# Kernel optimization log

Hardware: AMD Instinct MI355X
Metric: run time of the kernel (lower is better)

## Reference

```python
import jax, jax.numpy as jnp
import numpy as np

CL1_K = 25
CL2_K = 25


def cheb_stack(L, x0, K):
    # x0: (V, M) -> (K, V, M) Chebyshev basis T_k(L) x0
    if K == 1:
        return x0[None]
    x1 = L @ x0
    if K == 2:
        return jnp.stack([x0, x1])

    def step(carry, _):
        xm1, xm2 = carry
        xk = 2.0 * (L @ xm1) - xm2
        return (xk, xm1), xk

    _, rest = jax.lax.scan(step, (x1, x0), None, length=K - 2)
    return jnp.concatenate([x0[None], x1[None], rest], axis=0)


def graph_conv(x, L, W, b, K):
    # x: (B, C, V) -> (B, Fout, V); matches torch Graph_Conv permute/view logic
    B, C, V = x.shape
    x0 = x.transpose(2, 1, 0).reshape(V, C * B)
    xs = cheb_stack(L, x0, K)                              # (K, V, C*B)
    xs = xs.reshape(K, V, C, B).transpose(3, 1, 2, 0)      # (B, V, C, K)
    xs = xs.reshape(B * V, C * K)
    y = xs @ W.T + b                                       # (B*V, Fout)
    return y.reshape(B, V, -1).transpose(0, 2, 1)


def maxpool4(x):
    B, C, V = x.shape
    return x.reshape(B, C, V // 4, 4).max(axis=-1)


def setup_inputs() -> dict:
    key = jax.random.key(0)
    ks = jax.random.split(key, 10)
    B, C, V, Vp = 32, 16, 4000, 4096
    CL1_F, CL2_F, FC_F = 64, 128, 10
    x = jax.random.normal(ks[0], (B, C, V), dtype=jnp.float32)
    perm = jax.random.permutation(ks[1], Vp)
    # rescaled Laplacians, scaled for stable 25-step recurrence
    L1 = jax.random.normal(ks[2], (Vp, Vp), dtype=jnp.float32) * (0.3 / np.sqrt(Vp))
    L2 = jax.random.normal(ks[3], (Vp // 4, Vp // 4), dtype=jnp.float32) * (0.3 / np.sqrt(Vp // 4))
    W1 = jax.random.normal(ks[4], (CL1_F, C * CL1_K), dtype=jnp.float32) * np.sqrt(2.0 / (C * CL1_K + CL1_F))
    b1 = jnp.zeros((CL1_F,), dtype=jnp.float32)
    W2 = jax.random.normal(ks[5], (CL2_F, CL1_F * CL2_K), dtype=jnp.float32) * np.sqrt(2.0 / (CL1_F * CL2_K + CL2_F))
    b2 = jnp.zeros((CL2_F,), dtype=jnp.float32)
    FC_IN = CL2_F * Vp // 16
    Wfc = jax.random.normal(ks[6], (FC_F, FC_IN), dtype=jnp.float32) * np.sqrt(2.0 / (FC_IN + FC_F))
    bfc = jnp.zeros((FC_F,), dtype=jnp.float32)
    return {"x": x, "perm": perm, "L1": L1, "L2": L2, "W1": W1, "b1": b1,
            "W2": W2, "b2": b2, "Wfc": Wfc, "bfc": bfc}


def reference(x, perm, L1, L2, W1, b1, W2, b2, Wfc, bfc):
    # BatchNorm1d(affine=False), training-mode batch statistics
    mu = x.mean(axis=(0, 2), keepdims=True)
    var = x.var(axis=(0, 2), keepdims=True)
    x = (x - mu) / jnp.sqrt(var + 1e-5)
    # Permute: zero-pad vertices to len(perm), then index
    B, C, V = x.shape
    Vp = perm.shape[0]
    x = jnp.pad(x, ((0, 0), (0, 0), (0, Vp - V)))[:, :, perm]
    x = jax.nn.relu(graph_conv(x, L1, W1, b1, CL1_K))
    x = maxpool4(x)
    x = jax.nn.relu(graph_conv(x, L2, W2, b2, CL2_K))
    x = maxpool4(x)
    x = x.reshape(B, -1)
    # dropout in eval mode (identity)
    return x @ Wfc.T + bfc
```

## Files before the change

kernel.cpp:

```cpp
#include <hip/hip_runtime.h>

typedef _Float16 half8 __attribute__((ext_vector_type(8)));
typedef _Float16 half4 __attribute__((ext_vector_type(4)));
typedef float f32x4 __attribute__((ext_vector_type(4)));

__device__ __forceinline__ void gload_lds16(const void* g, void* l) {
  __builtin_amdgcn_global_load_lds((const __attribute__((address_space(1))) void*)g,
                                   (__attribute__((address_space(3))) void*)l, 16, 0, 0);
}

__global__ __launch_bounds__(256) void k_bn_partial(const float* __restrict__ x,
                                                    float* __restrict__ part) {
  const int c = blockIdx.x & 15;
  const int seg = blockIdx.x >> 4;
  const int t = threadIdx.x;
  float s = 0.f, s2 = 0.f;
  for (int b = 0; b < 32; ++b) {
    const float* row = x + (size_t)(b * 16 + c) * 4000 + seg * 500;
    for (int v = t; v < 500; v += 256) {
      float val = row[v];
      s += val;
      s2 += val * val;
    }
  }
#pragma unroll
  for (int off = 32; off > 0; off >>= 1) {
    s += __shfl_down(s, off);
    s2 += __shfl_down(s2, off);
  }
  __shared__ float rs_[4], rs2_[4];
  if ((t & 63) == 0) { rs_[t >> 6] = s; rs2_[t >> 6] = s2; }
  __syncthreads();
  if (t == 0) {
    part[c * 8 + seg] = rs_[0] + rs_[1] + rs_[2] + rs_[3];
    part[128 + c * 8 + seg] = rs2_[0] + rs2_[1] + rs2_[2] + rs2_[3];
  }
}

__global__ void k_bn_final(const float* __restrict__ part, float* __restrict__ musig) {
  const int c = threadIdx.x;
  if (c < 16) {
    float S = 0.f, S2 = 0.f;
#pragma unroll
    for (int seg = 0; seg < 8; ++seg) {
      S += part[c * 8 + seg];
      S2 += part[128 + c * 8 + seg];
    }
    const float inv = 1.f / 128000.f;
    float mu = S * inv;
    float var = S2 * inv - mu * mu;
    musig[c] = mu;
    musig[16 + c] = rsqrtf(var + 1e-5f);
  }
}

__global__ __launch_bounds__(256) void k_build_x0(const float* __restrict__ x,
                                                  const int* __restrict__ perm,
                                                  const float* __restrict__ musig,
                                                  _Float16* __restrict__ X0) {
  const int idx = blockIdx.x * 256 + threadIdx.x;
  const int v = idx & 4095;
  const int m = idx >> 12;
  const int b = m & 31;
  const int c = m >> 5;
  const int pv = perm[v];
  float val = 0.f;
  if (pv < 4000)
    val = (x[((size_t)(b * 16 + c)) * 4000 + pv] - musig[c]) * musig[16 + c] * 0.0625f;
  X0[idx] = (_Float16)val;
}

__global__ __launch_bounds__(256) void k_cvt_f16(const float* __restrict__ s,
                                                 _Float16* __restrict__ d, int n) {
  const int i = (blockIdx.x * 256 + threadIdx.x) * 4;
  if (i >= n) return;
  f32x4 v = *(const f32x4*)(s + i);
  half4 h;
  h[0] = (_Float16)v[0]; h[1] = (_Float16)v[1];
  h[2] = (_Float16)v[2]; h[3] = (_Float16)v[3];
  *(half4*)(d + i) = h;
}

__global__ __launch_bounds__(256) void k_zero(_Float16* __restrict__ p, int n8) {
  const int i = blockIdx.x * 256 + threadIdx.x;
  if (i < n8) *(half8*)(p + (size_t)i * 8) = half8{};
}

__global__ __launch_bounds__(256) void k_prep_w(const float* __restrict__ W,
                                                _Float16* __restrict__ Wp,
                                                int F, int shiftC, int kround) {
  const int idx = blockIdx.x * 256 + threadIdx.x;
  const int CS = 1 << shiftC;
  const int KPtot = kround * CS;
  if (idx >= F * KPtot) return;
  const int f = idx / KPtot;
  const int rem = idx - f * KPtot;
  const int k = rem >> shiftC;
  const int c = rem & (CS - 1);
  float v = 0.f;
  if (k < 25) v = W[(size_t)f * (CS * 25) + c * 25 + k];
  Wp[idx] = (_Float16)v;
}

__global__ __launch_bounds__(256, 2) void k_cheb1b(const _Float16* __restrict__ Xprev,
                                                   const _Float16* __restrict__ Lm,
                                                   _Float16* __restrict__ P) {
  __shared__ _Float16 lds[3][8192];
  const int t = threadIdx.x;
  const int lane = t & 63;
  const int ln = lane & 15;
  const int g = lane >> 4;
  const int w = t >> 6;
  const int wm = w >> 1, wn = w & 1;
  const int bid = blockIdx.x;
  const int kq = bid & 3;
  const int bx = (bid >> 2) & 31;
  const int by = bid >> 7;
  const int v0 = bx * 128, m0 = by * 128;
  const size_t rs = 8192;

  const char* Ag = (const char*)Xprev + (size_t)m0 * rs + kq * 2048;
  const char* Bg = (const char*)Lm + (size_t)v0 * rs + kq * 2048;

  f32x4 acc[4][4] = {};

  auto stage = [&](int buf, int tt) {
    char* A = (char*)&lds[buf][0];
    char* B = (char*)&lds[buf][4096];
#pragma unroll
    for (int j = 0; j < 2; ++j) {
      const int ch = j * 256 + t;
      const int row = ch >> 2, c8 = ch & 3;
      const size_t so = (size_t)row * rs + tt * 64 + ((c8 ^ ((row >> 1) & 3)) << 4);
      gload_lds16(Ag + so, A + ch * 16);
      gload_lds16(Bg + so, B + ch * 16);
    }
  };

  stage(0, 0);
  stage(1, 1);
  asm volatile("s_waitcnt vmcnt(4)" ::: "memory");
  asm volatile("s_barrier" ::: "memory");

  for (int tt = 0; tt < 32; ++tt) {
    const int cur = tt % 3;
    const char* A = (const char*)&lds[cur][0];
    const char* B = A + 8192;
    half8 a[4], b[4];
#pragma unroll
    for (int mi = 0; mi < 4; ++mi) {
      const int ar = wm * 64 + mi * 16 + ln;
      a[mi] = *(const half8*)(A + ar * 64 + ((g ^ ((ar >> 1) & 3)) << 4));
    }
#pragma unroll
    for (int ni = 0; ni < 4; ++ni) {
      const int br = wn * 64 + ni * 16 + ln;
      b[ni] = *(const half8*)(B + br * 64 + ((g ^ ((br >> 1) & 3)) << 4));
    }
    if (tt + 2 < 32) {
      stage((tt + 2) % 3, tt + 2);
      asm volatile("s_waitcnt vmcnt(4)" ::: "memory");
    } else {
      asm volatile("s_waitcnt vmcnt(0)" ::: "memory");
    }
    asm volatile("s_barrier" ::: "memory");
    asm volatile("s_waitcnt lgkmcnt(0)" ::: "memory");
    __builtin_amdgcn_sched_barrier(0);
    __builtin_amdgcn_s_setprio(1);
#pragma unroll
    for (int mi = 0; mi < 4; ++mi)
#pragma unroll
      for (int ni = 0; ni < 4; ++ni)
        acc[mi][ni] = __builtin_amdgcn_mfma_f32_16x16x32_f16(a[mi], b[ni], acc[mi][ni], 0, 0, 0);
    __builtin_amdgcn_s_setprio(0);
    asm volatile("s_barrier" ::: "memory");
  }

  _Float16* Pq = P + (size_t)kq * 2097152;
#pragma unroll
  for (int mi = 0; mi < 4; ++mi) {
#pragma unroll
    for (int ni = 0; ni < 4; ++ni) {
      const int vv = v0 + wn * 64 + ni * 16 + ln;
      const int mmb = m0 + wm * 64 + mi * 16 + g * 4;
#pragma unroll
      for (int r = 0; r < 4; ++r)
        Pq[(size_t)(mmb + r) * 4096 + vv] = (_Float16)acc[mi][ni][r];
    }
  }
}

__global__ __launch_bounds__(256) void k_cheb_red4(const _Float16* __restrict__ P,
                                                   const _Float16* __restrict__ Xm2,
                                                   _Float16* __restrict__ Xout,
                                                   float alpha, float beta) {
  const size_t i = ((size_t)blockIdx.x * 256 + threadIdx.x) * 8;
  float s[8] = {};
#pragma unroll
  for (int p = 0; p < 4; ++p) {
    half8 v = *(const half8*)(P + (size_t)p * 2097152 + i);
#pragma unroll
    for (int j = 0; j < 8; ++j) s[j] += (float)v[j];
  }
  half8 xm2 = {};
  if (beta != 0.f) xm2 = *(const half8*)(Xm2 + i);
  half8 o;
#pragma unroll
  for (int j = 0; j < 8; ++j) o[j] = (_Float16)(alpha * s[j] - beta * (float)xm2[j]);
  *(half8*)(Xout + i) = o;
}

__global__ __launch_bounds__(256, 2) void k_cheb2(const _Float16* __restrict__ Xprev,
                                                  const _Float16* __restrict__ Lm,
                                                  const _Float16* __restrict__ Xm2,
                                                  _Float16* __restrict__ Xout,
                                                  float alpha, float beta) {
  __shared__ _Float16 lds[3][8192];
  const int t = threadIdx.x;
  const int lane = t & 63;
  const int ln = lane & 15;
  const int g = lane >> 4;
  const int g16 = g << 4;
  const int w = t >> 6;
  const int wm = w >> 1, wn = w & 1;
  const int bx = blockIdx.x & 15;
  const int by = blockIdx.x >> 4;
  const int v0 = bx * 64, m0 = by * 64;
  const size_t rs = 2048;

  const char* Ag = (const char*)Xprev + (size_t)m0 * rs;
  const char* Bg = (const char*)Lm + (size_t)v0 * rs;

  f32x4 acc[2][2] = {};

  auto stageHalf = [&](int buf, int tt, int half) {
    const char* src = (half == 0) ? Ag : Bg;
    char* dst0 = (char*)&lds[buf][0] + half * 8192;
#pragma unroll
    for (int j = 0; j < 2; ++j) {
      const int idx = j * 256 + t;
      const int row = idx >> 3, c8 = idx & 7;
      gload_lds16(src + (size_t)row * rs + tt * 128 + ((c8 ^ (row & 7)) << 4),
                  dst0 + idx * 16);
    }
  };

  stageHalf(0, 0, 0); stageHalf(0, 0, 1);
  stageHalf(1, 1, 0); stageHalf(1, 1, 1);
  asm volatile("s_waitcnt vmcnt(4)" ::: "memory");
  asm volatile("s_barrier" ::: "memory");

  for (int tt = 0; tt < 16; ++tt) {
    const int cur = tt % 3;
    const int nxt = (tt + 2) % 3;
    const char* A = (const char*)&lds[cur][0];
    const char* B = A + 8192;
    half8 a[2][2], b[2][2];
#pragma unroll
    for (int kk = 0; kk < 2; ++kk) {
#pragma unroll
      for (int mi = 0; mi < 2; ++mi) {
        const int ar = wm * 32 + mi * 16 + ln;
        a[kk][mi] = *(const half8*)(A + ar * 128 + ((kk * 64 + g16) ^ ((ar & 7) << 4)));
      }
#pragma unroll
      for (int ni = 0; ni < 2; ++ni) {
        const int br = wn * 32 + ni * 16 + ln;
        b[kk][ni] = *(const half8*)(B + br * 128 + ((kk * 64 + g16) ^ ((br & 7) << 4)));
      }
    }
    if (tt + 2 < 16) {
      stageHalf(nxt, tt + 2, 0);
      stageHalf(nxt, tt + 2, 1);
      asm volatile("s_waitcnt vmcnt(4)" ::: "memory");
    } else {
      asm volatile("s_waitcnt vmcnt(0)" ::: "memory");
    }
    asm volatile("s_barrier" ::: "memory");
    asm volatile("s_waitcnt lgkmcnt(0)" ::: "memory");
    __builtin_amdgcn_sched_barrier(0);
    __builtin_amdgcn_s_setprio(1);
#pragma unroll
    for (int kk = 0; kk < 2; ++kk)
#pragma unroll
      for (int mi = 0; mi < 2; ++mi)
#pragma unroll
        for (int ni = 0; ni < 2; ++ni)
          acc[mi][ni] = __builtin_amdgcn_mfma_f32_16x16x32_f16(a[kk][mi], b[kk][ni],
                                                               acc[mi][ni], 0, 0, 0);
    __builtin_amdgcn_s_setprio(0);
    asm volatile("s_barrier" ::: "memory");
  }

#pragma unroll
  for (int mi = 0; mi < 2; ++mi) {
#pragma unroll
    for (int ni = 0; ni < 2; ++ni) {
      const int vv = v0 + wn * 32 + ni * 16 + ln;
      const int mmb = m0 + wm * 32 + mi * 16 + g * 4;
#pragma unroll
      for (int r = 0; r < 4; ++r) {
        const size_t idx = (size_t)(mmb + r) * 1024 + vv;
        float val = alpha * acc[mi][ni][r];
        if (beta != 0.f) val -= (float)Xm2[idx];
        Xout[idx] = (_Float16)val;
      }
    }
  }
}

template <int FT>
__global__ __launch_bounds__(256, 2) void k_dense(const _Float16* __restrict__ Wp,
                                                  const _Float16* __restrict__ XS,
                                                  const float* __restrict__ bias,
                                                  float* __restrict__ Yt,
                                                  int Vv, int shiftC, int nsteps,
                                                  int Ntot, float ascale, float bscale) {
  __shared__ _Float16 Alds[2][FT * 64];
  __shared__ _Float16 Blds[2][64 * 64];
  const int t = threadIdx.x;
  const int lane = t & 63;
  const int g = lane >> 4;
  const int w = t >> 6;
  const int n0 = blockIdx.x * 64;
  const int b = n0 / Vv;
  const int vb = n0 % Vv;
  const int Kp = nsteps * 64;
  const int cmask = (1 << shiftC) - 1;
  const size_t plane = 2097152;

  f32x4 acc[FT / 16] = {};

  auto stage = [&](int buf, int s) {
    const int q0 = s * 64;
    char* A = (char*)&Alds[buf][0];
    char* B = (char*)&Blds[buf][0];
#pragma unroll
    for (int j = 0; j < FT / 32; ++j) {
      const int ch = j * 256 + t;
      const int f = ch >> 3, c8 = ch & 7;
      gload_lds16((const char*)Wp + ((size_t)f * Kp + q0) * 2 + ((c8 ^ (f & 7)) << 4),
                  A + ch * 16);
    }
#pragma unroll
    for (int j = 0; j < 2; ++j) {
      const int ch = j * 256 + t;
      const int q = ch >> 3, c8 = ch & 7;
      const int qq = q0 + q;
      const int k = qq >> shiftC, c = qq & cmask;
      const int sz = (q >> 3) & 7;
      gload_lds16((const char*)XS + ((size_t)k * plane + (size_t)(c * 32 + b) * Vv + vb) * 2 +
                      ((c8 ^ sz) << 4),
                  B + ch * 16);
    }
  };

  stage(0, 0);

  for (int s = 0; s < nsteps; ++s) {
    const int cur = s & 1;
    if (s + 1 < nsteps) {
      stage(cur ^ 1, s + 1);
      if constexpr (FT == 64) {
        asm volatile("s_waitcnt vmcnt(4)" ::: "memory");
      } else {
        asm volatile("s_waitcnt vmcnt(6)" ::: "memory");
      }
    } else {
      asm volatile("s_waitcnt vmcnt(0)" ::: "memory");
    }
    asm volatile("s_barrier" ::: "memory");
    const _Float16* A = &Alds[cur][0];
    const _Float16* B = &Blds[cur][0];
#pragma unroll
    for (int kk = 0; kk < 2; ++kk) {
      half8 bf;
      const int c = lane & 15;
#pragma unroll
      for (int j = 0; j < 8; ++j) {
        const int q = kk * 32 + g * 8 + j;
        const int sz = (q >> 3) & 7;
        bf[j] = B[q * 64 + ((w * 16 + c) ^ (sz << 3))];
      }
#pragma unroll
      for (int mi = 0; mi < FT / 16; ++mi) {
        const int ar = mi * 16 + c;
        half8 af = *(const half8*)((const char*)A + ar * 128 +
                                   ((kk * 64 + g * 16) ^ ((ar & 7) << 4)));
        acc[mi] = __builtin_amdgcn_mfma_f32_16x16x32_f16(af, bf, acc[mi], 0, 0, 0);
      }
    }
    asm volatile("s_barrier" ::: "memory");
  }

  const int n = n0 + w * 16 + (lane & 15);
#pragma unroll
  for (int mi = 0; mi < FT / 16; ++mi) {
#pragma unroll
    for (int r = 0; r < 4; ++r) {
      const int f = mi * 16 + g * 4 + r;
      Yt[(size_t)f * Ntot + n] = fmaxf(ascale * acc[mi][r] + bscale * bias[f], 0.f);
    }
  }
}

__global__ __launch_bounds__(256) void k_pool1(const float* __restrict__ Yt,
                                               _Float16* __restrict__ X2) {
  const int idx = blockIdx.x * 256 + threadIdx.x;
  const int v2 = idx & 1023;
  const int rest = idx >> 10;
  const int b = rest & 31;
  const int f = rest >> 5;
  f32x4 q = *(const f32x4*)(Yt + (size_t)f * 131072 + b * 4096 + v2 * 4);
  float mx = fmaxf(fmaxf(q[0], q[1]), fmaxf(q[2], q[3]));
  X2[(size_t)(f * 32 + b) * 1024 + v2] = (_Float16)(mx * 0.015625f);
}

__global__ __launch_bounds__(256) void k_pool2(const float* __restrict__ Yt,
                                               float* __restrict__ p2) {
  const int idx = blockIdx.x * 256 + threadIdx.x;
  const int v3 = idx & 255;
  const int rest = idx >> 8;
  const int f = rest & 127;
  const int b = rest >> 7;
  f32x4 q = *(const f32x4*)(Yt + (size_t)f * 32768 + b * 1024 + v3 * 4);
  float mx = fmaxf(fmaxf(q[0], q[1]), fmaxf(q[2], q[3]));
  p2[(size_t)b * 32768 + f * 256 + v3] = mx;
}

__global__ __launch_bounds__(256) void k_fc_part(const float* __restrict__ p2,
                                                 const float* __restrict__ Wfc,
                                                 float* __restrict__ partF) {
  const int b = blockIdx.x >> 3;
  const int seg = blockIdx.x & 7;
  const int t = threadIdx.x;
  const int lane = t & 63;
  const int w = t >> 6;
  const int base = seg * 4096;
  float acc[10];
#pragma unroll
  for (int o = 0; o < 10; ++o) acc[o] = 0.f;
  const float* pb = p2 + (size_t)b * 32768 + base;
  for (int i = t; i < 4096; i += 256) {
    float p = pb[i];
#pragma unroll
    for (int o = 0; o < 10; ++o) acc[o] += p * Wfc[(size_t)o * 32768 + base + i];
  }
#pragma unroll
  for (int off = 32; off > 0; off >>= 1)
#pragma unroll
    for (int o = 0; o < 10; ++o) acc[o] += __shfl_down(acc[o], off);
  __shared__ float rws[10][4];
  if (lane == 0) {
#pragma unroll
    for (int o = 0; o < 10; ++o) rws[o][w] = acc[o];
  }
  __syncthreads();
  if (t < 10) partF[blockIdx.x * 10 + t] =
      rws[t][0] + rws[t][1] + rws[t][2] + rws[t][3];
}

__global__ void k_fc_final(const float* __restrict__ partF,
                           const float* __restrict__ bfc,
                           float* __restrict__ out) {
  const int t = threadIdx.x;
  if (t < 320) {
    const int b = t / 10, o = t - b * 10;
    float s = 0.f;
#pragma unroll
    for (int seg = 0; seg < 8; ++seg) s += partF[(b * 8 + seg) * 10 + o];
    out[b * 10 + o] = 64.f * s + bfc[o];
  }
}

extern "C" void kernel_launch(void* const* d_in, const int* in_sizes, int n_in,
                              void* d_out, int out_size, void* d_ws, size_t ws_size,
                              hipStream_t stream) {
  (void)in_sizes; (void)n_in; (void)out_size; (void)ws_size;
  const float* x = (const float*)d_in[0];
  const int* perm = (const int*)d_in[1];
  const float* L1 = (const float*)d_in[2];
  const float* L2 = (const float*)d_in[3];
  const float* W1 = (const float*)d_in[4];
  const float* b1 = (const float*)d_in[5];
  const float* W2 = (const float*)d_in[6];
  const float* b2 = (const float*)d_in[7];
  const float* Wfc = (const float*)d_in[8];
  const float* bfc = (const float*)d_in[9];
  float* out = (float*)d_out;

  char* ws = (char*)d_ws;
  size_t off = 0;
  auto alloc = [&](size_t bytes) {
    char* p = ws + off;
    off += (bytes + 255) & ~(size_t)255;
    return p;
  };
  _Float16* L1h = (_Float16*)alloc(16777216ull * 2);
  _Float16* L2h = (_Float16*)alloc(1048576ull * 2);
  _Float16* W1p = (_Float16*)alloc(64ull * 448 * 2);
  _Float16* W2p = (_Float16*)alloc(128ull * 1664 * 2);
  float* part = (float*)alloc(256 * 4);
  float* musig = (float*)alloc(32 * 4);
  float* partF = (float*)alloc(2560 * 4);
  _Float16* XS = (_Float16*)alloc(28ull * 2097152 * 2);
  float* Yt = (float*)alloc(64ull * 131072 * 4);
  float* p2 = (float*)alloc(32ull * 128 * 256 * 4);
  _Float16* Pq = (_Float16*)Yt;

  const size_t plane = 2097152;

  k_cvt_f16<<<16384, 256, 0, stream>>>(L1, L1h, 16777216);
  k_cvt_f16<<<1024, 256, 0, stream>>>(L2, L2h, 1048576);
  k_prep_w<<<112, 256, 0, stream>>>(W1, W1p, 64, 4, 28);
  k_prep_w<<<832, 256, 0, stream>>>(W2, W2p, 128, 6, 26);
  k_zero<<<3072, 256, 0, stream>>>(XS + 25 * plane, 786432);
  k_bn_partial<<<128, 256, 0, stream>>>(x, part);
  k_bn_final<<<1, 64, 0, stream>>>(part, musig);
  k_build_x0<<<8192, 256, 0, stream>>>(x, perm, musig, XS);

  for (int k = 1; k < 25; ++k) {
    k_cheb1b<<<512, 256, 0, stream>>>(XS + (size_t)(k - 1) * plane, L1h, Pq);
    k_cheb_red4<<<1024, 256, 0, stream>>>(
        Pq, XS + (size_t)(k >= 2 ? k - 2 : 0) * plane, XS + (size_t)k * plane,
        (k == 1) ? 1.f : 2.f, (k == 1) ? 0.f : 1.f);
  }
  k_dense<64><<<dim3(2048, 1), 256, 0, stream>>>(W1p, XS, b1, Yt, 4096, 4, 7,
                                                 131072, 16.f, 1.f);
  k_pool1<<<8192, 256, 0, stream>>>(Yt, XS);
  for (int k = 1; k < 25; ++k) {
    k_cheb2<<<512, 256, 0, stream>>>(
        XS + (size_t)(k - 1) * plane, L2h,
        XS + (size_t)(k >= 2 ? k - 2 : 0) * plane, XS + (size_t)k * plane,
        (k == 1) ? 1.f : 2.f, (k == 1) ? 0.f : 1.f);
  }
  k_dense<128><<<dim3(512, 1), 256, 0, stream>>>(W2p, XS, b2, Yt, 1024, 6, 26,
                                                 32768, 1.f, 0.015625f);
  k_pool2<<<4096, 256, 0, stream>>>(Yt, p2);
  k_fc_part<<<256, 256, 0, stream>>>(p2, Wfc, partF);
  k_fc_final<<<1, 320, 0, stream>>>(partF, bfc, out);
}
```

Baseline: 1.188 ms.

## Fuse maxpool into dense epilogue and deepen cheb1 LDS pipeline to four stages

The dense kernels now apply the 4-way max pool in their epilogue with lane shuffles and write pooled outputs directly. This removes the separate pool kernels and the full-resolution fp32 intermediate writes and reads. The layer-1 pooled output goes to a new extra plane so it doesn't clobber plane 0 while it is still being read. Separately, the cheb1 GEMM uses four LDS buffers with a prefetch distance of three to hide more global-load latency, at the cost of more shared memory per block.

```diff
diff --git a/kernel.cpp b/kernel.cpp
--- a/kernel.cpp
+++ b/kernel.cpp
@@ -105,7 +105,7 @@
 __global__ __launch_bounds__(256, 2) void k_cheb1b(const _Float16* __restrict__ Xprev,
                                                    const _Float16* __restrict__ Lm,
                                                    _Float16* __restrict__ P) {
-  __shared__ _Float16 lds[3][8192];
+  __shared__ _Float16 lds[4][8192];
   const int t = threadIdx.x;
   const int lane = t & 63;
   const int ln = lane & 15;
@@ -139,11 +139,12 @@
 
   stage(0, 0);
   stage(1, 1);
-  asm volatile("s_waitcnt vmcnt(4)" ::: "memory");
+  stage(2, 2);
+  asm volatile("s_waitcnt vmcnt(8)" ::: "memory");
   asm volatile("s_barrier" ::: "memory");
 
   for (int tt = 0; tt < 32; ++tt) {
-    const int cur = tt % 3;
+    const int cur = tt & 3;
     const char* A = (const char*)&lds[cur][0];
     const char* B = A + 8192;
     half8 a[4], b[4];
@@ -157,8 +158,10 @@
       const int br = wn * 64 + ni * 16 + ln;
       b[ni] = *(const half8*)(B + br * 64 + ((g ^ ((br >> 1) & 3)) << 4));
     }
-    if (tt + 2 < 32) {
-      stage((tt + 2) % 3, tt + 2);
+    if (tt + 3 < 32) {
+      stage((tt + 3) & 3, tt + 3);
+      asm volatile("s_waitcnt vmcnt(8)" ::: "memory");
+    } else if (tt + 2 < 32) {
       asm volatile("s_waitcnt vmcnt(4)" ::: "memory");
     } else {
       asm volatile("s_waitcnt vmcnt(0)" ::: "memory");
@@ -309,13 +312,13 @@
   }
 }
 
-template <int FT>
+template <int FT, int MODE>
 __global__ __launch_bounds__(256, 2) void k_dense(const _Float16* __restrict__ Wp,
                                                   const _Float16* __restrict__ XS,
                                                   const float* __restrict__ bias,
-                                                  float* __restrict__ Yt,
+                                                  void* __restrict__ outp,
                                                   int Vv, int shiftC, int nsteps,
-                                                  int Ntot, float ascale, float bscale) {
+                                                  int k0plane, float ascale, float bscale) {
   __shared__ _Float16 Alds[2][FT * 64];
   __shared__ _Float16 Blds[2][64 * 64];
   const int t = threadIdx.x;
@@ -347,7 +350,9 @@
       const int ch = j * 256 + t;
       const int q = ch >> 3, c8 = ch & 7;
       const int qq = q0 + q;
-      const int k = qq >> shiftC, c = qq & cmask;
+      int k = qq >> shiftC;
+      const int c = qq & cmask;
+      if (k == 0) k = k0plane;
       const int sz = (q >> 3) & 7;
       gload_lds16((const char*)XS + ((size_t)k * plane + (size_t)(c * 32 + b) * Vv + vb) * 2 +
                       ((c8 ^ sz) << 4),
@@ -393,39 +398,27 @@
     asm volatile("s_barrier" ::: "memory");
   }
 
-  const int n = n0 + w * 16 + (lane & 15);
+  const int v = vb + w * 16 + (lane & 15);
+  const bool writer = (lane & 3) == 0;
 #pragma unroll
   for (int mi = 0; mi < FT / 16; ++mi) {
 #pragma unroll
     for (int r = 0; r < 4; ++r) {
       const int f = mi * 16 + g * 4 + r;
-      Yt[(size_t)f * Ntot + n] = fmaxf(ascale * acc[mi][r] + bscale * bias[f], 0.f);
-    }
-  }
-}
-
-__global__ __launch_bounds__(256) void k_pool1(const float* __restrict__ Yt,
-                                               _Float16* __restrict__ X2) {
-  const int idx = blockIdx.x * 256 + threadIdx.x;
-  const int v2 = idx & 1023;
-  const int rest = idx >> 10;
-  const int b = rest & 31;
-  const int f = rest >> 5;
-  f32x4 q = *(const f32x4*)(Yt + (size_t)f * 131072 + b * 4096 + v2 * 4);
-  float mx = fmaxf(fmaxf(q[0], q[1]), fmaxf(q[2], q[3]));
-  X2[(size_t)(f * 32 + b) * 1024 + v2] = (_Float16)(mx * 0.015625f);
-}
-
-__global__ __launch_bounds__(256) void k_pool2(const float* __restrict__ Yt,
-                                               float* __restrict__ p2) {
-  const int idx = blockIdx.x * 256 + threadIdx.x;
-  const int v3 = idx & 255;
-  const int rest = idx >> 8;
-  const int f = rest & 127;
-  const int b = rest >> 7;
-  f32x4 q = *(const f32x4*)(Yt + (size_t)f * 32768 + b * 1024 + v3 * 4);
-  float mx = fmaxf(fmaxf(q[0], q[1]), fmaxf(q[2], q[3]));
-  p2[(size_t)b * 32768 + f * 256 + v3] = mx;
+      float val = fmaxf(ascale * acc[mi][r] + bscale * bias[f], 0.f);
+      val = fmaxf(val, __shfl_xor(val, 1));
+      val = fmaxf(val, __shfl_xor(val, 2));
+      if (writer) {
+        if constexpr (MODE == 1) {
+          _Float16* Xp = (_Float16*)outp;
+          Xp[(size_t)(f * 32 + b) * 1024 + (v >> 2)] = (_Float16)(val * 0.015625f);
+        } else {
+          float* p2 = (float*)outp;
+          p2[(size_t)b * 32768 + f * 256 + (v >> 2)] = val;
+        }
+      }
+    }
+  }
 }
 
 __global__ __launch_bounds__(256) void k_fc_part(const float* __restrict__ p2,
@@ -503,7 +496,7 @@
   float* part = (float*)alloc(256 * 4);
   float* musig = (float*)alloc(32 * 4);
   float* partF = (float*)alloc(2560 * 4);
-  _Float16* XS = (_Float16*)alloc(28ull * 2097152 * 2);
+  _Float16* XS = (_Float16*)alloc(29ull * 2097152 * 2);
   float* Yt = (float*)alloc(64ull * 131072 * 4);
   float* p2 = (float*)alloc(32ull * 128 * 256 * 4);
   _Float16* Pq = (_Float16*)Yt;
@@ -525,18 +518,16 @@
         Pq, XS + (size_t)(k >= 2 ? k - 2 : 0) * plane, XS + (size_t)k * plane,
         (k == 1) ? 1.f : 2.f, (k == 1) ? 0.f : 1.f);
   }
-  k_dense<64><<<dim3(2048, 1), 256, 0, stream>>>(W1p, XS, b1, Yt, 4096, 4, 7,
-                                                 131072, 16.f, 1.f);
-  k_pool1<<<8192, 256, 0, stream>>>(Yt, XS);
+  k_dense<64, 1><<<dim3(2048, 1), 256, 0, stream>>>(W1p, XS, b1, XS + 28 * plane,
+                                                    4096, 4, 7, 0, 16.f, 1.f);
+  auto Xp = [&](int k) { return XS + (size_t)((k == 0) ? 28 : k) * plane; };
   for (int k = 1; k < 25; ++k) {
     k_cheb2<<<512, 256, 0, stream>>>(
-        XS + (size_t)(k - 1) * plane, L2h,
-        XS + (size_t)(k >= 2 ? k - 2 : 0) * plane, XS + (size_t)k * plane,
+        Xp(k - 1), L2h, Xp(k >= 2 ? k - 2 : 0), Xp(k),
         (k == 1) ? 1.f : 2.f, (k == 1) ? 0.f : 1.f);
   }
-  k_dense<128><<<dim3(512, 1), 256, 0, stream>>>(W2p, XS, b2, Yt, 1024, 6, 26,
-                                                 32768, 1.f, 0.015625f);
-  k_pool2<<<4096, 256, 0, stream>>>(Yt, p2);
+  k_dense<128, 2><<<dim3(512, 1), 256, 0, stream>>>(W2p, XS, b2, p2,
+                                                    1024, 6, 26, 28, 1.f, 0.015625f);
   k_fc_part<<<256, 256, 0, stream>>>(p2, Wfc, partF);
   k_fc_final<<<1, 320, 0, stream>>>(partF, bfc, out);
 }
```

Measured after the change: 1.169 ms. About the same (-1.6%).
